# Kernel tuning notes

Measured on AMD Instinct MI355X. Metric: run time of the kernel, lower is better.

The kernel has to match this reference:

```python
import jax, jax.numpy as jnp
import numpy as np

B, N_OBJ, K, D_MSG = 1024, 128, 32, 64
Y0 = 0.28209479177387814  # 1/(2*sqrt(pi)), l=0 integral-normalized SH
Y1 = 0.4886025119029199   # sqrt(3/(4*pi)),  l=1 integral-normalized SH


def _sh_lmax1(vec):
    """Spherical harmonics up to l=1, normalize=True, 'integral' normalization. [...,3] -> [...,4]."""
    r = jnp.linalg.norm(vec, axis=-1, keepdims=True)
    u = vec / jnp.maximum(r, 1e-12)
    return jnp.concatenate([jnp.full_like(r, Y0), Y1 * u], axis=-1)


def _forward(inputs, W_msg, W_out):
    Bsz, n, _ = inputs.shape
    masses = inputs[..., 0:1]           # [B,n,1]
    loc = inputs[..., 1:4]              # [B,n,3]
    vel = inputs[..., 4:7]              # [B,n,3]
    # canonicalize_mode == 'com': weights = masses
    w = masses
    com = jnp.sum(w / jnp.sum(w, axis=-2, keepdims=True) * loc, axis=-2, keepdims=True)
    loc = loc - com
    # --- knn_graph per batch element (loop=False, k nearest excluding self) ---
    d2 = jnp.sum((loc[:, :, None, :] - loc[:, None, :, :]) ** 2, axis=-1)  # [B,n,n]
    d2 = jnp.where(jnp.eye(n, dtype=bool)[None], jnp.inf, d2)
    _, nbr = jax.lax.top_k(-d2, K)                                          # [B,n,K]
    offs = (jnp.arange(Bsz) * n)[:, None, None]
    src = (nbr + offs).reshape(-1)                                          # edge_index[0]: neighbor j
    dst = (jnp.broadcast_to(jnp.arange(n)[None, :, None], (Bsz, n, K)) + offs).reshape(-1)  # edge_index[1]: center i
    # --- flatten node tensors ---
    pos = loc.reshape(-1, 3)
    v = vel.reshape(-1, 3)
    m = masses.reshape(-1, 1)
    Nn = Bsz * n
    # --- gravity graph augmentation ---
    rel = pos[src] - pos[dst]
    edge_dist = jnp.linalg.norm(rel, axis=-1, keepdims=True)
    prod_mass = m[src] * m[dst]
    edge_attr = _sh_lmax1(rel)                                              # [E,4]
    vel_emb = _sh_lmax1(v)                                                  # [Nn,4]
    deg = jnp.maximum(jax.ops.segment_sum(jnp.ones(src.shape[0], jnp.float32), dst, num_segments=Nn), 1.0)[:, None]
    node_attr = jax.ops.segment_sum(edge_attr, dst, num_segments=Nn) / deg + vel_emb
    vel_abs = jnp.linalg.norm(v, axis=-1, keepdims=True)
    x = jnp.concatenate([pos, v, vel_abs], axis=-1)                         # [Nn,7]
    amf = jnp.concatenate([edge_dist, prod_mass], axis=-1)                  # [E,2]
    # --- surrogate SEGNN: one message-passing layer ---
    m_in = jnp.concatenate([x[src], x[dst], edge_attr, amf], axis=-1)       # [E,20]
    msg = jax.nn.relu(m_in @ W_msg)                                         # [E,64]
    agg = jax.ops.segment_sum(msg, dst, num_segments=Nn) / deg              # [Nn,64]
    pred_shift = jnp.concatenate([x, node_attr, agg], axis=-1) @ W_out      # [Nn,3]
    return loc + pred_shift.reshape(Bsz, n, 3) + com


def setup_inputs() -> dict:
    key = jax.random.key(0)
    k1, k2, k3 = jax.random.split(key, 3)
    inputs = jax.random.uniform(k1, (B, N_OBJ, 7), dtype=jnp.float32)  # positive masses in col 0
    W_msg = jax.random.normal(k2, (20, D_MSG), dtype=jnp.float32) * 0.1
    W_out = jax.random.normal(k3, (D_MSG + 7 + 4, 3), dtype=jnp.float32) * 0.1
    return {"inputs": inputs, "W_msg": W_msg, "W_out": W_out}


def reference(inputs, W_msg, W_out):
    pred = _forward(inputs, W_msg, W_out)
    return (pred, jnp.zeros(inputs.shape[0], dtype=jnp.float32))
```

## Files before the change

kernel.cpp:

```cpp
#include <hip/hip_runtime.h>

#define NB 1024
#define NN 128
#define KK 32
#define DM 64

constexpr float Y0 = 0.28209479177387814f;
constexpr float Y1 = 0.4886025119029199f;


__global__ __launch_bounds__(128) void k1_prep(const float* __restrict__ in,
        float* __restrict__ feats, float* __restrict__ com, float* __restrict__ out)
{
    const int b = blockIdx.x, t = threadIdx.x;
    const float* p = in + ((size_t)b*NN + t)*7;
    const float m  = p[0];
    const float lx = p[1], ly = p[2], lz = p[3];
    const float vx = p[4], vy = p[5], vz = p[6];
    float w=m, wx=m*lx, wy=m*ly, wz=m*lz;
    #pragma unroll
    for (int s=1; s<64; s<<=1) {
        w  += __shfl_xor(w,  s);
        wx += __shfl_xor(wx, s);
        wy += __shfl_xor(wy, s);
        wz += __shfl_xor(wz, s);
    }
    __shared__ float red[2][4];
    if ((t & 63) == 0) { int wi=t>>6; red[wi][0]=w; red[wi][1]=wx; red[wi][2]=wy; red[wi][3]=wz; }
    __syncthreads();
    const float Wt = red[0][0]+red[1][0];
    const float cx = (red[0][1]+red[1][1])/Wt;
    const float cy = (red[0][2]+red[1][2])/Wt;
    const float cz = (red[0][3]+red[1][3])/Wt;
    const float px = lx-cx, py = ly-cy, pz = lz-cz;
    const float va = sqrtf(vx*vx+vy*vy+vz*vz);
    float4* f4 = (float4*)(feats + ((size_t)b*NN + t)*8);
    f4[0] = make_float4(px,py,pz,vx);
    f4[1] = make_float4(vy,vz,va,m);
    if (t==0) { float4* c4=(float4*)(com + (size_t)b*4); *c4 = make_float4(cx,cy,cz,0.f); }
    if (b < 8) out[(size_t)NB*NN*3 + (size_t)b*128 + t] = 0.f;
}

__global__ __launch_bounds__(256) void k2_knn(const float* __restrict__ feats,
                                              int* __restrict__ nbr)
{
    const int b = blockIdx.x, t = threadIdx.x;
    const int lane = t & 63, w = t >> 6;
    __shared__ float4 sP[128];
    if (t < 128) sP[t] = *(const float4*)(feats + ((size_t)b*NN + t)*8);
    __syncthreads();
    const float4 A4 = sP[lane];
    const float4 B4 = sP[lane+64];
    const float INF = __int_as_float(0x7f800000);
    const unsigned long long lt = (1ULL<<lane)-1ULL;
    #pragma unroll 1
    for (int i=0; i<32; i+=2) {
        const int n0 = w*32 + i, n1 = n0+1;
        const float4 C0 = sP[n0], C1 = sP[n1];
        float dx,dy,dz;
        dx=A4.x-C0.x; dy=A4.y-C0.y; dz=A4.z-C0.z;
        float d2a0 = dx*dx+dy*dy+dz*dz;
        dx=B4.x-C0.x; dy=B4.y-C0.y; dz=B4.z-C0.z;
        float d2b0 = dx*dx+dy*dy+dz*dz;
        dx=A4.x-C1.x; dy=A4.y-C1.y; dz=A4.z-C1.z;
        float d2a1 = dx*dx+dy*dy+dz*dz;
        dx=B4.x-C1.x; dy=B4.y-C1.y; dz=B4.z-C1.z;
        float d2b1 = dx*dx+dy*dy+dz*dz;
        if (lane    == n0) d2a0 = INF;
        if (lane+64 == n0) d2b0 = INF;
        if (lane    == n1) d2a1 = INF;
        if (lane+64 == n1) d2b1 = INF;
        const unsigned ua0=__float_as_uint(d2a0), ub0=__float_as_uint(d2b0);
        const unsigned ua1=__float_as_uint(d2a1), ub1=__float_as_uint(d2b1);
        unsigned P0=0u, P1=0u;
        #pragma unroll 1
        for (int bit=30;bit>=0;--bit) {
            const unsigned Q0=P0|(1u<<bit), Q1=P1|(1u<<bit);
            const int c0 = __popcll(__ballot(ua0<Q0)) + __popcll(__ballot(ub0<Q0));
            const int c1 = __popcll(__ballot(ua1<Q1)) + __popcll(__ballot(ub1<Q1));
            if (c0<=31) P0=Q0;
            if (c1<=31) P1=Q1;
        }
        {
            const unsigned long long m0=__ballot(ua0<P0), m1=__ballot(ub0<P0);
            const unsigned long long e0=__ballot(ua0==P0), e1=__ballot(ub0==P0);
            const int c0n=__popcll(m0), c=c0n+__popcll(m1), rem=32-c;
            int* row = nbr + ((size_t)b*NN + n0)*32;
            if (ua0< P0) row[__popcll(m0&lt)] = lane;
            if (ub0< P0) row[c0n+__popcll(m1&lt)] = lane+64;
            if (ua0==P0) { const int r=__popcll(e0&lt);               if (r<rem) row[c+r]=lane; }
            if (ub0==P0) { const int r=__popcll(e0)+__popcll(e1&lt);  if (r<rem) row[c+r]=lane+64; }
        }
        {
            const unsigned long long m0=__ballot(ua1<P1), m1=__ballot(ub1<P1);
            const unsigned long long e0=__ballot(ua1==P1), e1=__ballot(ub1==P1);
            const int c0n=__popcll(m0), c=c0n+__popcll(m1), rem=32-c;
            int* row = nbr + ((size_t)b*NN + n1)*32;
            if (ua1< P1) row[__popcll(m0&lt)] = lane;
            if (ub1< P1) row[c0n+__popcll(m1&lt)] = lane+64;
            if (ua1==P1) { const int r=__popcll(e0&lt);               if (r<rem) row[c+r]=lane; }
            if (ub1==P1) { const int r=__popcll(e0)+__popcll(e1&lt);  if (r<rem) row[c+r]=lane+64; }
        }
    }
}

__global__ __launch_bounds__(256) void k3_main(const float* __restrict__ feats,
        const int* __restrict__ nbr, const float* __restrict__ Wm,
        const float* __restrict__ Wo, const float* __restrict__ com,
        float* __restrict__ out)
{
    const int b = blockIdx.x, t = threadIdx.x;
    __shared__ float4 sPos[128];
    __shared__ float4 sVel[128];
    __shared__ __align__(16) float sXs[128*64];
    __shared__ float  sWm[20][64];
    __shared__ float  sWo[75][3];
    __shared__ float4 sE4[32][33];
    __shared__ float  sPm[32][33];
    __shared__ int    sSrc[32][33];
    __shared__ float4 sSu[32];

    for (int i=t;i<1280;i+=256) ((float*)sWm)[i] = Wm[i];
    for (int i=t;i<225; i+=256) ((float*)sWo)[i] = Wo[i];
    if (t < 128) {
        const float4* f4 = (const float4*)(feats + ((size_t)b*NN + t)*8);
        sPos[t] = f4[0];
        sVel[t] = f4[1];
    }
    __syncthreads();
    if (t < 128) {
        const float4 a = sPos[t], c = sVel[t];
        sPos[t] = make_float4(a.x,a.y,a.z,c.w);
        sVel[t] = make_float4(a.w,c.x,c.y,c.z);
    }
    __syncthreads();

    for (int i=t;i<8192;i+=256) {
        const int n = i>>6, d = i&63;
        const float4 P = sPos[n], V = sVel[n];
        float s = P.x*sWm[0][d];
        s = fmaf(P.y, sWm[1][d], s);
        s = fmaf(P.z, sWm[2][d], s);
        s = fmaf(V.x, sWm[3][d], s);
        s = fmaf(V.y, sWm[4][d], s);
        s = fmaf(V.z, sWm[5][d], s);
        s = fmaf(V.w, sWm[6][d], s);
        const int q = d>>2;
        sXs[(n<<6) + ((q ^ (n&7))<<2) + (d&3)] = s;
    }
    __syncthreads();

    const int dsub = t & 7, ng = t >> 3, d0 = dsub*8, q0 = dsub*2;
    float wc[5][8];
    #pragma unroll
    for (int r=0;r<5;r++)
        #pragma unroll
        for (int c=0;c<8;c++) wc[r][c] = sWm[15+r][d0+c];
    const float cmx = com[(size_t)b*4+0], cmy = com[(size_t)b*4+1], cmz = com[(size_t)b*4+2];

    #pragma unroll 1
    for (int ch=0; ch<4; ++ch) {
        {
            const int nl = t>>3, j0 = (t&7)*4;
            const int n  = ch*32 + nl;
            const float4 Pn = sPos[n];
            const int4 nb4 = *(const int4*)(nbr + ((size_t)b*NN + n)*32 + j0);
            const int js[4] = {nb4.x, nb4.y, nb4.z, nb4.w};
            float sx=0.f, sy=0.f, sz=0.f;
            #pragma unroll
            for (int r=0;r<4;r++) {
                const int s = js[r];
                const float4 Ps = sPos[s];
                const float rx=Ps.x-Pn.x, ry=Ps.y-Pn.y, rz=Ps.z-Pn.z;
                const float dist = sqrtf(rx*rx+ry*ry+rz*rz);
                const float inv  = Y1 * __builtin_amdgcn_rcpf(fmaxf(dist,1e-12f));
                const float ux=rx*inv, uy=ry*inv, uz=rz*inv;
                sx+=ux; sy+=uy; sz+=uz;
                sE4[nl][j0+r] = make_float4(ux,uy,uz,dist);
                sPm[nl][j0+r] = Ps.w*Pn.w;
                sSrc[nl][j0+r] = s;
            }
            #pragma unroll
            for (int s=1;s<8;s<<=1) { sx+=__shfl_xor(sx,s); sy+=__shfl_xor(sy,s); sz+=__shfl_xor(sz,s); }
            if ((t&7)==0) sSu[nl] = make_float4(sx,sy,sz,0.f);
        }
        __syncthreads();

        {
            const int n = ch*32 + ng;
            const float4 Pn = sPos[n], Vn = sVel[n];
            float xdb[8];
            #pragma unroll
            for (int c=0;c<8;c++) {
                float s = Y0 * sWm[14][d0+c];
                s = fmaf(Pn.x, sWm[7][d0+c], s);
                s = fmaf(Pn.y, sWm[8][d0+c], s);
                s = fmaf(Pn.z, sWm[9][d0+c], s);
                s = fmaf(Vn.x, sWm[10][d0+c], s);
                s = fmaf(Vn.y, sWm[11][d0+c], s);
                s = fmaf(Vn.z, sWm[12][d0+c], s);
                s = fmaf(Vn.w, sWm[13][d0+c], s);
                xdb[c] = s;
            }
            float acc[8];
            #pragma unroll
            for (int c=0;c<8;c++) acc[c]=0.f;
            #pragma unroll 8
            for (int e=0;e<32;e++) {
                const float4 E = sE4[ng][e];
                const float pm = sPm[ng][e];
                const int s = sSrc[ng][e];
                const int a0 = (s<<8) + ((q0 ^ (s&7))<<4);
                const float4 xsA = *(const float4*)((const char*)sXs + a0);
                const float4 xsB = *(const float4*)((const char*)sXs + (a0^16));
                const float xs[8] = {xsA.x,xsA.y,xsA.z,xsA.w, xsB.x,xsB.y,xsB.z,xsB.w};
                #pragma unroll
                for (int c=0;c<8;c++) {
                    float v = xdb[c] + xs[c];
                    v = fmaf(E.x, wc[0][c], v);
                    v = fmaf(E.y, wc[1][c], v);
                    v = fmaf(E.z, wc[2][c], v);
                    v = fmaf(E.w, wc[3][c], v);
                    v = fmaf(pm,  wc[4][c], v);
                    acc[c] += fmaxf(v, 0.f);
                }
            }
            float p0=0.f,p1=0.f,p2=0.f;
            #pragma unroll
            for (int c=0;c<8;c++) {
                const float a = acc[c]*(1.0f/32.0f);
                p0 = fmaf(a, sWo[11+d0+c][0], p0);
                p1 = fmaf(a, sWo[11+d0+c][1], p1);
                p2 = fmaf(a, sWo[11+d0+c][2], p2);
            }
            #pragma unroll
            for (int s=1;s<8;s<<=1) {
                p0 += __shfl_xor(p0,s); p1 += __shfl_xor(p1,s); p2 += __shfl_xor(p2,s);
            }
            if (dsub == 0) {
                const float4 Su = sSu[ng];
                const float vinv = Y1 * __builtin_amdgcn_rcpf(fmaxf(Vn.w,1e-12f));
                const float na0 = 2.f*Y0;
                const float na1 = Su.x*(1.f/32.f) + Vn.x*vinv;
                const float na2 = Su.y*(1.f/32.f) + Vn.y*vinv;
                const float na3 = Su.z*(1.f/32.f) + Vn.z*vinv;
                const float xf[7] = {Pn.x,Pn.y,Pn.z,Vn.x,Vn.y,Vn.z,Vn.w};
                #pragma unroll
                for (int k=0;k<7;k++) {
                    p0 = fmaf(xf[k], sWo[k][0], p0);
                    p1 = fmaf(xf[k], sWo[k][1], p1);
                    p2 = fmaf(xf[k], sWo[k][2], p2);
                }
                p0 += na0*sWo[7][0] + na1*sWo[8][0] + na2*sWo[9][0] + na3*sWo[10][0];
                p1 += na0*sWo[7][1] + na1*sWo[8][1] + na2*sWo[9][1] + na3*sWo[10][1];
                p2 += na0*sWo[7][2] + na1*sWo[8][2] + na2*sWo[9][2] + na3*sWo[10][2];
                float* op = out + ((size_t)b*NN + n)*3;
                op[0] = Pn.x + cmx + p0;
                op[1] = Pn.y + cmy + p1;
                op[2] = Pn.z + cmz + p2;
            }
        }
        __syncthreads();
    }
}

extern "C" void kernel_launch(void* const* d_in, const int* in_sizes, int n_in,
                              void* d_out, int out_size, void* d_ws, size_t ws_size,
                              hipStream_t stream)
{
    const float* in = (const float*)d_in[0];
    const float* Wm = (const float*)d_in[1];
    const float* Wo = (const float*)d_in[2];
    float* out = (float*)d_out;
    float* feats = (float*)d_ws;
    float* com   = feats + (size_t)NB*NN*8;
    int*   nbr   = (int*)(com + (size_t)NB*4);

    k1_prep<<<NB, 128, 0, stream>>>(in, feats, com, out);
    k2_knn <<<NB, 256, 0, stream>>>(feats, nbr);
    k3_main<<<NB, 256, 0, stream>>>(feats, nbr, Wm, Wo, com, out);
}
```

Before: 219.2 us.

## Fuse prep into kNN kernel, batch four radix selects, pack message math as float2

Merges the center-of-mass prep kernel into the kNN kernel so positions go straight to shared memory, saving one launch and a global round trip. The kNN radix-select now handles four query nodes per iteration instead of two, giving more independent ballots to hide latency at the cost of more registers. The message MLP inner loop in the main kernel uses 2-wide float vectors so the compiler can emit packed FMA/max instructions. The zeroing of the second output now writes one element per block instead of 128 per block for the first 8 blocks; both cover the same 1024 entries.

```diff
diff --git a/kernel.cpp b/kernel.cpp
--- a/kernel.cpp
+++ b/kernel.cpp
@@ -8,98 +8,91 @@
 constexpr float Y0 = 0.28209479177387814f;
 constexpr float Y1 = 0.4886025119029199f;
 
-
-__global__ __launch_bounds__(128) void k1_prep(const float* __restrict__ in,
-        float* __restrict__ feats, float* __restrict__ com, float* __restrict__ out)
-{
-    const int b = blockIdx.x, t = threadIdx.x;
-    const float* p = in + ((size_t)b*NN + t)*7;
-    const float m  = p[0];
-    const float lx = p[1], ly = p[2], lz = p[3];
-    const float vx = p[4], vy = p[5], vz = p[6];
-    float w=m, wx=m*lx, wy=m*ly, wz=m*lz;
-    #pragma unroll
-    for (int s=1; s<64; s<<=1) {
-        w  += __shfl_xor(w,  s);
-        wx += __shfl_xor(wx, s);
-        wy += __shfl_xor(wy, s);
-        wz += __shfl_xor(wz, s);
-    }
-    __shared__ float red[2][4];
-    if ((t & 63) == 0) { int wi=t>>6; red[wi][0]=w; red[wi][1]=wx; red[wi][2]=wy; red[wi][3]=wz; }
-    __syncthreads();
-    const float Wt = red[0][0]+red[1][0];
-    const float cx = (red[0][1]+red[1][1])/Wt;
-    const float cy = (red[0][2]+red[1][2])/Wt;
-    const float cz = (red[0][3]+red[1][3])/Wt;
-    const float px = lx-cx, py = ly-cy, pz = lz-cz;
-    const float va = sqrtf(vx*vx+vy*vy+vz*vz);
-    float4* f4 = (float4*)(feats + ((size_t)b*NN + t)*8);
-    f4[0] = make_float4(px,py,pz,vx);
-    f4[1] = make_float4(vy,vz,va,m);
-    if (t==0) { float4* c4=(float4*)(com + (size_t)b*4); *c4 = make_float4(cx,cy,cz,0.f); }
-    if (b < 8) out[(size_t)NB*NN*3 + (size_t)b*128 + t] = 0.f;
-}
-
-__global__ __launch_bounds__(256) void k2_knn(const float* __restrict__ feats,
-                                              int* __restrict__ nbr)
+typedef float f2 __attribute__((ext_vector_type(2)));
+
+
+__global__ __launch_bounds__(256) void k12_prep_knn(const float* __restrict__ in,
+        float* __restrict__ feats, float* __restrict__ com, int* __restrict__ nbr,
+        float* __restrict__ out)
 {
     const int b = blockIdx.x, t = threadIdx.x;
     const int lane = t & 63, w = t >> 6;
     __shared__ float4 sP[128];
-    if (t < 128) sP[t] = *(const float4*)(feats + ((size_t)b*NN + t)*8);
-    __syncthreads();
+    __shared__ float red[2][4];
+
+    float m=0.f,lx=0.f,ly=0.f,lz=0.f,vx=0.f,vy=0.f,vz=0.f;
+    if (t < 128) {
+        const float* p = in + ((size_t)b*NN + t)*7;
+        m=p[0]; lx=p[1]; ly=p[2]; lz=p[3]; vx=p[4]; vy=p[5]; vz=p[6];
+    }
+    {
+        float sw=m, sx=m*lx, sy=m*ly, sz=m*lz;
+        #pragma unroll
+        for (int s=1;s<64;s<<=1) {
+            sw+=__shfl_xor(sw,s); sx+=__shfl_xor(sx,s);
+            sy+=__shfl_xor(sy,s); sz+=__shfl_xor(sz,s);
+        }
+        if (t<128 && lane==0) { red[w][0]=sw; red[w][1]=sx; red[w][2]=sy; red[w][3]=sz; }
+    }
+    if (t==0) out[(size_t)NB*NN*3 + b] = 0.f;
+    __syncthreads();
+    const float Wt  = red[0][0]+red[1][0];
+    const float cmx = (red[0][1]+red[1][1])/Wt;
+    const float cmy = (red[0][2]+red[1][2])/Wt;
+    const float cmz = (red[0][3]+red[1][3])/Wt;
+    if (t < 128) {
+        const float px=lx-cmx, py=ly-cmy, pz=lz-cmz;
+        const float va = sqrtf(vx*vx+vy*vy+vz*vz);
+        sP[t] = make_float4(px,py,pz,m);
+        float4* f4 = (float4*)(feats + ((size_t)b*NN + t)*8);
+        f4[0] = make_float4(px,py,pz,vx);
+        f4[1] = make_float4(vy,vz,va,m);
+        if (t==0) { float4* c4=(float4*)(com + (size_t)b*4); *c4 = make_float4(cmx,cmy,cmz,0.f); }
+    }
+    __syncthreads();
+
     const float4 A4 = sP[lane];
     const float4 B4 = sP[lane+64];
     const float INF = __int_as_float(0x7f800000);
     const unsigned long long lt = (1ULL<<lane)-1ULL;
     #pragma unroll 1
-    for (int i=0; i<32; i+=2) {
-        const int n0 = w*32 + i, n1 = n0+1;
-        const float4 C0 = sP[n0], C1 = sP[n1];
-        float dx,dy,dz;
-        dx=A4.x-C0.x; dy=A4.y-C0.y; dz=A4.z-C0.z;
-        float d2a0 = dx*dx+dy*dy+dz*dz;
-        dx=B4.x-C0.x; dy=B4.y-C0.y; dz=B4.z-C0.z;
-        float d2b0 = dx*dx+dy*dy+dz*dz;
-        dx=A4.x-C1.x; dy=A4.y-C1.y; dz=A4.z-C1.z;
-        float d2a1 = dx*dx+dy*dy+dz*dz;
-        dx=B4.x-C1.x; dy=B4.y-C1.y; dz=B4.z-C1.z;
-        float d2b1 = dx*dx+dy*dy+dz*dz;
-        if (lane    == n0) d2a0 = INF;
-        if (lane+64 == n0) d2b0 = INF;
-        if (lane    == n1) d2a1 = INF;
-        if (lane+64 == n1) d2b1 = INF;
-        const unsigned ua0=__float_as_uint(d2a0), ub0=__float_as_uint(d2b0);
-        const unsigned ua1=__float_as_uint(d2a1), ub1=__float_as_uint(d2b1);
-        unsigned P0=0u, P1=0u;
+    for (int i=0; i<32; i+=4) {
+        const int nb0 = w*32 + i;
+        unsigned ua[4], ub[4], P[4];
+        #pragma unroll
+        for (int k=0;k<4;k++) {
+            const int n = nb0 + k;
+            const float4 C = sP[n];
+            float dx=A4.x-C.x, dy=A4.y-C.y, dz=A4.z-C.z;
+            float d2a = dx*dx+dy*dy+dz*dz;
+            dx=B4.x-C.x; dy=B4.y-C.y; dz=B4.z-C.z;
+            float d2b = dx*dx+dy*dy+dz*dz;
+            if (lane    == n) d2a = INF;
+            if (lane+64 == n) d2b = INF;
+            ua[k]=__float_as_uint(d2a); ub[k]=__float_as_uint(d2b);
+            P[k]=0u;
+        }
         #pragma unroll 1
         for (int bit=30;bit>=0;--bit) {
-            const unsigned Q0=P0|(1u<<bit), Q1=P1|(1u<<bit);
-            const int c0 = __popcll(__ballot(ua0<Q0)) + __popcll(__ballot(ub0<Q0));
-            const int c1 = __popcll(__ballot(ua1<Q1)) + __popcll(__ballot(ub1<Q1));
-            if (c0<=31) P0=Q0;
-            if (c1<=31) P1=Q1;
-        }
-        {
-            const unsigned long long m0=__ballot(ua0<P0), m1=__ballot(ub0<P0);
-            const unsigned long long e0=__ballot(ua0==P0), e1=__ballot(ub0==P0);
+            const unsigned msk = 1u<<bit;
+            #pragma unroll
+            for (int k=0;k<4;k++) {
+                const unsigned Q = P[k]|msk;
+                const int cnt = __popcll(__ballot(ua[k]<Q)) + __popcll(__ballot(ub[k]<Q));
+                if (cnt<=31) P[k]=Q;
+            }
+        }
+        #pragma unroll
+        for (int k=0;k<4;k++) {
+            const unsigned T = P[k];
+            const unsigned long long m0=__ballot(ua[k]<T), m1=__ballot(ub[k]<T);
+            const unsigned long long e0=__ballot(ua[k]==T), e1=__ballot(ub[k]==T);
             const int c0n=__popcll(m0), c=c0n+__popcll(m1), rem=32-c;
-            int* row = nbr + ((size_t)b*NN + n0)*32;
-            if (ua0< P0) row[__popcll(m0&lt)] = lane;
-            if (ub0< P0) row[c0n+__popcll(m1&lt)] = lane+64;
-            if (ua0==P0) { const int r=__popcll(e0&lt);               if (r<rem) row[c+r]=lane; }
-            if (ub0==P0) { const int r=__popcll(e0)+__popcll(e1&lt);  if (r<rem) row[c+r]=lane+64; }
-        }
-        {
-            const unsigned long long m0=__ballot(ua1<P1), m1=__ballot(ub1<P1);
-            const unsigned long long e0=__ballot(ua1==P1), e1=__ballot(ub1==P1);
-            const int c0n=__popcll(m0), c=c0n+__popcll(m1), rem=32-c;
-            int* row = nbr + ((size_t)b*NN + n1)*32;
-            if (ua1< P1) row[__popcll(m0&lt)] = lane;
-            if (ub1< P1) row[c0n+__popcll(m1&lt)] = lane+64;
-            if (ua1==P1) { const int r=__popcll(e0&lt);               if (r<rem) row[c+r]=lane; }
-            if (ub1==P1) { const int r=__popcll(e0)+__popcll(e1&lt);  if (r<rem) row[c+r]=lane+64; }
+            int* row = nbr + ((size_t)b*NN + nb0 + k)*32;
+            if (ua[k]< T) row[__popcll(m0&lt)] = lane;
+            if (ub[k]< T) row[c0n+__popcll(m1&lt)] = lane+64;
+            if (ua[k]==T) { const int r=__popcll(e0&lt);               if (r<rem) row[c+r]=lane; }
+            if (ub[k]==T) { const int r=__popcll(e0)+__popcll(e1&lt);  if (r<rem) row[c+r]=lane+64; }
         }
     }
 }
@@ -151,11 +144,14 @@
     __syncthreads();
 
     const int dsub = t & 7, ng = t >> 3, d0 = dsub*8, q0 = dsub*2;
-    float wc[5][8];
+    f2 wc2[5][4];
     #pragma unroll
     for (int r=0;r<5;r++)
         #pragma unroll
-        for (int c=0;c<8;c++) wc[r][c] = sWm[15+r][d0+c];
+        for (int j=0;j<4;j++) {
+            wc2[r][j].x = sWm[15+r][d0+2*j];
+            wc2[r][j].y = sWm[15+r][d0+2*j+1];
+        }
     const float cmx = com[(size_t)b*4+0], cmy = com[(size_t)b*4+1], cmz = com[(size_t)b*4+2];
 
     #pragma unroll 1
@@ -189,22 +185,27 @@
         {
             const int n = ch*32 + ng;
             const float4 Pn = sPos[n], Vn = sVel[n];
-            float xdb[8];
-            #pragma unroll
-            for (int c=0;c<8;c++) {
-                float s = Y0 * sWm[14][d0+c];
-                s = fmaf(Pn.x, sWm[7][d0+c], s);
-                s = fmaf(Pn.y, sWm[8][d0+c], s);
-                s = fmaf(Pn.z, sWm[9][d0+c], s);
-                s = fmaf(Vn.x, sWm[10][d0+c], s);
-                s = fmaf(Vn.y, sWm[11][d0+c], s);
-                s = fmaf(Vn.z, sWm[12][d0+c], s);
-                s = fmaf(Vn.w, sWm[13][d0+c], s);
-                xdb[c] = s;
-            }
-            float acc[8];
-            #pragma unroll
-            for (int c=0;c<8;c++) acc[c]=0.f;
+            f2 xdb2[4];
+            #pragma unroll
+            for (int j=0;j<4;j++) {
+                #pragma unroll
+                for (int h=0;h<2;h++) {
+                    const int c = 2*j+h;
+                    float s = Y0 * sWm[14][d0+c];
+                    s = fmaf(Pn.x, sWm[7][d0+c], s);
+                    s = fmaf(Pn.y, sWm[8][d0+c], s);
+                    s = fmaf(Pn.z, sWm[9][d0+c], s);
+                    s = fmaf(Vn.x, sWm[10][d0+c], s);
+                    s = fmaf(Vn.y, sWm[11][d0+c], s);
+                    s = fmaf(Vn.z, sWm[12][d0+c], s);
+                    s = fmaf(Vn.w, sWm[13][d0+c], s);
+                    if (h==0) xdb2[j].x = s; else xdb2[j].y = s;
+                }
+            }
+            f2 acc2[4];
+            #pragma unroll
+            for (int j=0;j<4;j++) acc2[j] = (f2){0.f,0.f};
+            const f2 zero2 = (f2){0.f,0.f};
             #pragma unroll 8
             for (int e=0;e<32;e++) {
                 const float4 E = sE4[ng][e];
@@ -213,25 +214,40 @@
                 const int a0 = (s<<8) + ((q0 ^ (s&7))<<4);
                 const float4 xsA = *(const float4*)((const char*)sXs + a0);
                 const float4 xsB = *(const float4*)((const char*)sXs + (a0^16));
-                const float xs[8] = {xsA.x,xsA.y,xsA.z,xsA.w, xsB.x,xsB.y,xsB.z,xsB.w};
+                f2 xs2[4];
+                xs2[0] = (f2){xsA.x, xsA.y};
+                xs2[1] = (f2){xsA.z, xsA.w};
+                xs2[2] = (f2){xsB.x, xsB.y};
+                xs2[3] = (f2){xsB.z, xsB.w};
+                const f2 ex = (f2){E.x, E.x};
+                const f2 ey = (f2){E.y, E.y};
+                const f2 ez = (f2){E.z, E.z};
+                const f2 ew = (f2){E.w, E.w};
+                const f2 pm2 = (f2){pm, pm};
                 #pragma unroll
-                for (int c=0;c<8;c++) {
-                    float v = xdb[c] + xs[c];
-                    v = fmaf(E.x, wc[0][c], v);
-                    v = fmaf(E.y, wc[1][c], v);
-                    v = fmaf(E.z, wc[2][c], v);
-                    v = fmaf(E.w, wc[3][c], v);
-                    v = fmaf(pm,  wc[4][c], v);
-                    acc[c] += fmaxf(v, 0.f);
+                for (int j=0;j<4;j++) {
+                    f2 v = xdb2[j] + xs2[j];
+                    v = __builtin_elementwise_fma(ex,  wc2[0][j], v);
+                    v = __builtin_elementwise_fma(ey,  wc2[1][j], v);
+                    v = __builtin_elementwise_fma(ez,  wc2[2][j], v);
+                    v = __builtin_elementwise_fma(ew,  wc2[3][j], v);
+                    v = __builtin_elementwise_fma(pm2, wc2[4][j], v);
+                    v = __builtin_elementwise_max(v, zero2);
+                    acc2[j] += v;
                 }
             }
             float p0=0.f,p1=0.f,p2=0.f;
             #pragma unroll
-            for (int c=0;c<8;c++) {
-                const float a = acc[c]*(1.0f/32.0f);
-                p0 = fmaf(a, sWo[11+d0+c][0], p0);
-                p1 = fmaf(a, sWo[11+d0+c][1], p1);
-                p2 = fmaf(a, sWo[11+d0+c][2], p2);
+            for (int j=0;j<4;j++) {
+                const float a0v = acc2[j].x*(1.0f/32.0f);
+                const float a1v = acc2[j].y*(1.0f/32.0f);
+                const int c0 = 2*j, c1 = 2*j+1;
+                p0 = fmaf(a0v, sWo[11+d0+c0][0], p0);
+                p1 = fmaf(a0v, sWo[11+d0+c0][1], p1);
+                p2 = fmaf(a0v, sWo[11+d0+c0][2], p2);
+                p0 = fmaf(a1v, sWo[11+d0+c1][0], p0);
+                p1 = fmaf(a1v, sWo[11+d0+c1][1], p1);
+                p2 = fmaf(a1v, sWo[11+d0+c1][2], p2);
             }
             #pragma unroll
             for (int s=1;s<8;s<<=1) {
@@ -276,7 +292,6 @@
     float* com   = feats + (size_t)NB*NN*8;
     int*   nbr   = (int*)(com + (size_t)NB*4);
 
-    k1_prep<<<NB, 128, 0, stream>>>(in, feats, com, out);
-    k2_knn <<<NB, 256, 0, stream>>>(feats, nbr);
-    k3_main<<<NB, 256, 0, stream>>>(feats, nbr, Wm, Wo, com, out);
+    k12_prep_knn<<<NB, 256, 0, stream>>>(in, feats, com, nbr, out);
+    k3_main     <<<NB, 256, 0, stream>>>(feats, nbr, Wm, Wo, com, out);
 }
```

New measurement: 198.8 us. 9.3% less time.
